# Performance work log

Hardware: AMD Instinct MI355X
Metric: run time of the kernel (lower is better)

The kernel has to match this reference:

```python
import jax, jax.numpy as jnp
import numpy as np

V = 131072          # total vertices (hits) across all events
K = 64              # neighbours per vertex, col 0 == self
NSEG = 4            # number of events (row splits segments)
THRESHOLD = 0.5     # hierarchy score cut (layer's non-trainable threshold var)


def setup_inputs() -> dict:
    key = jax.random.key(0)
    k1, k2 = jax.random.split(key)
    score = jax.random.uniform(k1, (V, 1), dtype=jnp.float32)
    seg = V // NSEG
    base = (jnp.arange(V, dtype=jnp.int32) // seg) * seg
    # random neighbours constrained to the same segment; column 0 is self
    rnd = jax.random.randint(k2, (V, K - 1), 0, seg, dtype=jnp.int32) + base[:, None]
    nidxs = jnp.concatenate([jnp.arange(V, dtype=jnp.int32)[:, None], rnd], axis=1)
    row_splits = (jnp.arange(NSEG + 1, dtype=jnp.int32) * seg)
    return {"score": score, "nidxs": nidxs, "row_splits": row_splits}


def _local_group(score1, nidxs, row_splits, thr):
    """Greedy threshold-based neighbour grouping (HGCalML LocalGroup op).

    Vertices are visited per segment in descending score order. An unused
    vertex becomes a group seed; if its score > thr it absorbs all of its
    not-yet-used neighbours. Returns fixed-shape (-1 padded) outputs so the
    whole thing is jit-compatible.
    """
    V_, K_ = nidxs.shape
    seg_id = jnp.searchsorted(row_splits, jnp.arange(V_, dtype=row_splits.dtype),
                              side='right') - 1
    # per-segment descending-score order == tf.argsort(DESC) per row split
    order = jnp.lexsort((-score1, seg_id)).astype(jnp.int32)
    kcols = jnp.arange(K_)

    def step(state, v):
        used, assign, dirn, sel, seed, count = state
        is_new = jnp.logical_not(used[v])                 # v not grouped yet -> seed
        expand = score1[v] > thr                          # absorb neighbours?
        cand = jnp.where(expand, nidxs[v],
                         jnp.where(kcols == 0, v, -1))    # else only self
        safe = jnp.clip(cand, 0, V_ - 1)
        valid = (cand >= 0) & jnp.logical_not(used[safe]) & is_new
        used = used.at[safe].set(used[safe] | valid)
        assign = assign.at[safe].set(jnp.where(valid, count, assign[safe]))
        dirn = dirn.at[v].set(jnp.where(valid, cand, -1))
        sel = sel.at[count].set(jnp.where(is_new, v, sel[count]))
        seed = seed.at[v].set(seed[v] | is_new)
        count = count + is_new.astype(jnp.int32)
        return (used, assign, dirn, sel, seed, count), None

    init = (jnp.zeros(V_, dtype=bool),                 # used
            jnp.full(V_, -1, jnp.int32),               # backgather: seed rank per vertex
            jnp.full((V_, K_), -1, jnp.int32),         # directed neighbour idxs
            jnp.full(V_, -1, jnp.int32),               # selected seed vertices, -1 padded
            jnp.zeros(V_, dtype=bool),                 # seed mask
            jnp.int32(0))
    (used, assign, dirn, sel, seed, count), _ = jax.lax.scan(step, init, order)
    cs0 = jnp.concatenate([jnp.zeros(1, jnp.int32),
                           jnp.cumsum(seed.astype(jnp.int32))])
    rs_new = cs0[row_splits]                           # new row splits over seeds
    return rs_new, dirn, sel[:, None], assign, count


def reference(score, nidxs, row_splits):
    # layer: score = clip(score, 0, 1); per-segment argsort; LocalGroup
    score1 = jnp.clip(score.reshape(-1), 0.0, 1.0)
    rs_new, dirnidx, sel, backgather, n_sel = _local_group(score1, nidxs,
                                                           row_splits, THRESHOLD)
    # return_backscatter=True -> back = [V, sel]; we return sel (padded) + n_sel
    # outputs: directed nidx (V,K), selection idxs (V,1 padded with -1),
    #          backgather (V,), new row splits, number selected
    return dirnidx, sel, backgather, rs_new, n_sel
```

## Files before the change

### kernel.cpp

```cpp
#include <hip/hip_runtime.h>
#include <stdint.h>

#define INFU 0xFFFFFFFFu
#define LCAP 32768
#define NC 128

__global__ void __launch_bounds__(256) k_hist(const float* score, unsigned* bcnt,
                                              unsigned* claim, int* sel, int V, int SEGN){
  int v = blockIdx.x*blockDim.x+threadIdx.x; if (v>=V) return;
  claim[v]=INFU;
  sel[v]=-1;
  float s = score[v]; s = fminf(fmaxf(s,0.f),1.f);
  int b = (int)(s*(float)SEGN); if (b>=SEGN) b=SEGN-1; if (b<0) b=0;
  int bd = SEGN-1-b;
  int seg = v / SEGN;
  atomicAdd(&bcnt[(size_t)seg*SEGN+bd], 1u);
}

__global__ void __launch_bounds__(1024) k_scan(const unsigned* in, const unsigned* claim,
                                               unsigned* outExcl, unsigned* segTotal,
                                               int SEGN, int mode){
  int seg = blockIdx.x; int tid = threadIdx.x; int lane = tid&63, wv = tid>>6;
  __shared__ unsigned wsum[16];
  const int CH = (SEGN+1023)>>10;
  int i0 = tid*CH, i1 = i0+CH; if (i1>SEGN) i1=SEGN;
  const size_t base = (size_t)seg*SEGN;
  unsigned sum=0;
  for (int i=i0;i<i1;i++){
    unsigned x = (mode==0)? in[base+i] : ((claim[base+i]==INFU)?1u:0u);
    sum+=x;
  }
  unsigned incl=sum;
  for (int off=1;off<64;off<<=1){ unsigned t=__shfl_up(incl,(unsigned)off); if (lane>=off) incl+=t; }
  if (lane==63) wsum[wv]=incl;
  __syncthreads();
  unsigned wbase=0,total=0;
  for (int w=0;w<16;w++){ unsigned s=wsum[w]; if (w<wv) wbase+=s; total+=s; }
  unsigned run = wbase + incl - sum;
  for (int i=i0;i<i1;i++){
    unsigned x = (mode==0)? in[base+i] : ((claim[base+i]==INFU)?1u:0u);
    outExcl[base+i]=run; run+=x;
  }
  if (tid==0 && segTotal) segTotal[seg]=total;
}

__global__ void __launch_bounds__(256) k_scatter(const float* score, const unsigned* bbase,
                                                 unsigned* bfill, unsigned long long* slot,
                                                 int V, int SEGN){
  int v = blockIdx.x*blockDim.x+threadIdx.x; if (v>=V) return;
  float s = score[v]; s=fminf(fmaxf(s,0.f),1.f);
  int b=(int)(s*(float)SEGN); if(b>=SEGN)b=SEGN-1; if(b<0)b=0;
  int bd=SEGN-1-b; int seg=v/SEGN;
  size_t bk = (size_t)seg*SEGN+bd;
  unsigned pos = bbase[bk] + atomicAdd(&bfill[bk],1u);
  unsigned kb = ~__float_as_uint(s);
  slot[(size_t)seg*SEGN+pos] = ((unsigned long long)kb<<32) | (unsigned)v;
}

__global__ void __launch_bounds__(256) k_bsort(const unsigned* bcnt, const unsigned* bbase,
                                               unsigned long long* slot, int V, int SEGN){
  int t = blockIdx.x*blockDim.x+threadIdx.x; if (t>=V) return;
  unsigned n = bcnt[t];
  if (n<2) return;
  int seg = t / SEGN;
  unsigned long long* a = slot + (size_t)seg*SEGN + bbase[t];
  for (unsigned i=1;i<n;i++){
    unsigned long long key=a[i]; int j=(int)i-1;
    while (j>=0 && a[j]>key){ a[j+1]=a[j]; j--; }
    a[j+1]=key;
  }
}

__global__ void __launch_bounds__(256) k_build(const unsigned long long* slot,
                                               int* ord, unsigned* rnkv, int* segE,
                                               int V, int SEGN){
  int r = blockIdx.x*blockDim.x+threadIdx.x; if (r>=V) return;
  unsigned long long sl = slot[r];
  int v = (int)(unsigned)(sl & 0xFFFFFFFFull);
  ord[r]=v;
  int seg = r / SEGN; int rl = r - seg*SEGN;
  rnkv[v] = (unsigned)rl;
  float s = __uint_as_float(~(unsigned)(sl>>32));
  bool ex = (s > 0.5f);
  if (rl==0 && !ex) segE[seg]=0;
  if (ex){
    if (rl==SEGN-1) segE[seg]=SEGN;
    else {
      float s2 = __uint_as_float(~(unsigned)(slot[r+1]>>32));
      if (!(s2 > 0.5f)) segE[seg]=rl+1;
    }
  }
}

__global__ void __launch_bounds__(256) k_pack4(const int* ord, const unsigned* rnkv, const int* nidxs,
                                               const int* segE, unsigned short* nbr16,
                                               int V, int K, int SEGN){
  const int K4 = K>>2;
  long long q = (long long)blockIdx.x*256 + threadIdx.x;
  if (q >= (long long)V*K4) return;
  int gr = (int)(q / K4); int k4 = (int)(q - (long long)gr*K4);
  int seg = gr / SEGN, r = gr - seg*SEGN;
  if (r >= segE[seg]) return;
  int v = ord[gr];
  const int4 nn = *(const int4*)(nidxs + (size_t)v*K + (size_t)k4*4);
  ushort4 o;
  o.x=(unsigned short)rnkv[nn.x]; o.y=(unsigned short)rnkv[nn.y];
  o.z=(unsigned short)rnkv[nn.z]; o.w=(unsigned short)rnkv[nn.w];
  *(ushort4*)(nbr16 + (size_t)gr*K + (size_t)k4*4) = o;
}
__global__ void __launch_bounds__(256) k_pack(const int* ord, const unsigned* rnkv, const int* nidxs,
                                              const int* segE, unsigned short* nbr16,
                                              int V, int K, int SEGN){
  long long t = (long long)blockIdx.x*256 + threadIdx.x;
  if (t >= (long long)V*K) return;
  int gr = (int)(t / K); int k = (int)(t - (long long)gr*K);
  int seg = gr / SEGN, r = gr - seg*SEGN;
  if (r >= segE[seg]) return;
  int v = ord[gr];
  int w = nidxs[(size_t)v*K + k];
  nbr16[t] = (unsigned short)rnkv[w];
}

__global__ void __launch_bounds__(1024) k_greedy(const unsigned short* nbr16, const int* segE,
                                                 unsigned* claim, int SEGN, int K){
  __shared__ unsigned s_cl[LCAP/2];
  __shared__ unsigned char s_pos[LCAP];
  __shared__ unsigned s_cand[NC];
  __shared__ unsigned long long s_McLo[NC];
  __shared__ unsigned long long s_McHi[NC];
  __shared__ unsigned long long s_anyLo, s_anyHi;
  __shared__ unsigned long long s_bm[16];
  __shared__ unsigned s_wcur;
  __shared__ unsigned long long s_v0, s_v1;
  const int seg = blockIdx.x, tid = threadIdx.x, lane = tid&63, wv = tid>>6;
  unsigned* clg = claim + (size_t)seg*SEGN;
  const int E = segE[seg];
  const int cap = (LCAP < SEGN) ? LCAP : SEGN;
  const int capw = (cap+1)>>1;
  for (int i=tid; i<capw; i+=1024) s_cl[i]=0xFFFFFFFFu;
  for (int i=tid; i<((cap+3)>>2); i+=1024) ((unsigned*)s_pos)[i]=0u;
  if (tid<NC) s_cand[tid]=INFU;
  const unsigned long long lt_mask = (lane==0) ? 0ull : ((~0ull) >> (64-lane));
  unsigned wcursor = 0;
  for (;;){
    __syncthreads();
    if (tid<NC){
      unsigned pc = s_cand[tid];
      if (pc!=INFU && pc<(unsigned)cap) s_pos[pc]=0;
      s_cand[tid]=INFU; s_McLo[tid]=0ull; s_McHi[tid]=0ull;
    }
    if (tid==NC)   s_anyLo=0ull;
    if (tid==NC+1) s_anyHi=0ull;
    int found = 0;
    for (;;){
      unsigned r = wcursor + (unsigned)(wv*64 + lane);
      bool undec=false;
      if (r<(unsigned)E){
        if (r<(unsigned)cap)
          undec = (((s_cl[r>>1]>>((r&1)*16))&0xFFFFu)==0xFFFFu);
        else
          undec = (__hip_atomic_load(&clg[r], __ATOMIC_RELAXED, __HIP_MEMORY_SCOPE_AGENT)==INFU);
      }
      unsigned long long m = __ballot(undec);
      if (lane==0) s_bm[wv]=m;
      __syncthreads();
      unsigned long long mb = (lane<16)? s_bm[lane] : 0ull;
      int pc16 = (int)__popcll(mb);
      int incl = pc16;
      #pragma unroll
      for (int off=1; off<16; off<<=1){ int t=__shfl_up(incl,off); if (lane>=off) incl+=t; }
      int total = __shfl(incl, 15);
      int below = __shfl(incl, wv) - __shfl(pc16, wv);
      int pos = found + below + (int)__popcll(m & lt_mask);
      if (undec && pos<NC){
        s_cand[pos]=r;
        if (r<(unsigned)cap) s_pos[r]=(unsigned char)(pos+1);
      }
      if (undec && pos==NC-1) s_wcur=r+1;
      bool filled = (found+total>=NC);
      bool winend = (wcursor + 1024 >= (unsigned)E);
      __syncthreads();
      if (filled){ wcursor = s_wcur; found=NC; break; }
      found += total;
      if (winend){ wcursor=(unsigned)E; break; }
      wcursor += 1024;
    }
    const int ncand = found;
    if (!ncand) break;
    unsigned rwq[8], cq[8];
    #pragma unroll
    for (int q=0;q<8;q++){
      int c=(wv<<3)|q;
      cq[q] = (c<ncand) ? s_cand[c] : INFU;
    }
    #pragma unroll
    for (int q=0;q<8;q++){
      rwq[q]=INFU;
      if (cq[q]!=INFU && lane<K)
        rwq[q] = (unsigned)nbr16[((size_t)seg*SEGN + cq[q])*K + lane];
    }
    const bool fastmap = (s_cand[ncand-1] < (unsigned)cap);
    #pragma unroll
    for (int q=0;q<8;q++){
      int c=(wv<<3)|q;
      if (cq[q]!=INFU){
        unsigned rw = rwq[q];
        int p = -1;
        if (fastmap){
          if (rw<(unsigned)cap){ p = (int)s_pos[rw] - 1; }
        } else {
          int pp=0;
          if (s_cand[pp+64]<=rw) pp+=64;
          if (s_cand[pp+32]<=rw) pp+=32;
          if (s_cand[pp+16]<=rw) pp+=16;
          if (s_cand[pp+8 ]<=rw) pp+=8;
          if (s_cand[pp+4 ]<=rw) pp+=4;
          if (s_cand[pp+2 ]<=rw) pp+=2;
          if (s_cand[pp+1 ]<=rw) pp+=1;
          if (pp<ncand && s_cand[pp]==rw) p=pp;
        }
        if (lane<K && p>c){
          if (p<64){ atomicOr(&s_McLo[c], 1ull<<p);      atomicOr(&s_anyLo, 1ull<<p); }
          else     { atomicOr(&s_McHi[c], 1ull<<(p-64)); atomicOr(&s_anyHi, 1ull<<(p-64)); }
        }
      }
    }
    __syncthreads();
    if (wv==0){
      const int n0 = (ncand<64)? ncand : 64;
      const int n1 = ncand - n0;
      const unsigned long long nmask0 = (n0==64)? ~0ull : ((1ull<<n0)-1ull);
      unsigned long long Mj0 = s_McLo[lane];
      unsigned long long any0 = s_anyLo & nmask0;
      unsigned long long valid0 = (~any0) & nmask0;
      unsigned long long rem = any0;
      while (rem){
        int i=__builtin_ctzll(rem); rem &= rem-1;
        bool pred = ((valid0>>lane)&1ull) && (lane<i) && ((Mj0>>i)&1ull);
        if (__ballot(pred)==0ull) valid0 |= (1ull<<i);
      }
      unsigned long long valid1 = 0ull;
      if (n1>0){
        const unsigned long long nmask1 = (n1==64)? ~0ull : ((1ull<<n1)-1ull);
        unsigned long long sp = ((valid0>>lane)&1ull) ? s_McHi[lane] : 0ull;
        #pragma unroll
        for (int off=32; off; off>>=1)
          sp |= (unsigned long long)__shfl_xor((long long)sp, off);
        unsigned long long Mj1 = s_McHi[64+lane];
        unsigned long long any1 = s_anyHi & nmask1;
        valid1 = (~(any1|sp)) & nmask1;
        unsigned long long rem1 = any1 & ~sp;
        while (rem1){
          int i=__builtin_ctzll(rem1); rem1 &= rem1-1;
          bool pred = ((valid1>>lane)&1ull) && (lane<i) && ((Mj1>>i)&1ull);
          if (__ballot(pred)==0ull) valid1 |= (1ull<<i);
        }
      }
      if (lane==0){ s_v0=valid0; s_v1=valid1; }
    }
    __syncthreads();
    const unsigned long long v0 = s_v0, v1 = s_v1;
    #pragma unroll
    for (int q=0;q<8;q++){
      int c=(wv<<3)|q;
      bool isv = (c<64) ? (((v0>>c)&1ull)!=0ull) : (((v1>>(c-64))&1ull)!=0ull);
      if (cq[q]!=INFU && isv){
        unsigned rw=rwq[q], cr=cq[q];
        if (rw>cr && rw!=INFU){
          if (rw<(unsigned)cap){
            unsigned idx=rw>>1, sh=(rw&1)*16;
            unsigned old=s_cl[idx];
            for(;;){
              unsigned curv=(old>>sh)&0xFFFFu;
              if (cr>=curv) break;
              unsigned neu=(old & ~(0xFFFFu<<sh)) | (cr<<sh);
              unsigned prev=atomicCAS(&s_cl[idx], old, neu);
              if (prev==old) break;
              old=prev;
            }
          } else {
            atomicMin(&clg[rw], cr);
          }
        }
      }
    }
  }
  __syncthreads();
  for (int r=tid; r<cap; r+=1024){
    unsigned c=(s_cl[r>>1]>>((r&1)*16))&0xFFFFu;
    clg[r] = (c==0xFFFFu) ? INFU : c;
  }
}

__global__ void __launch_bounds__(256) k_absorb(const unsigned* rnkv, const unsigned* claim,
                                                unsigned* absorb, int V, int SEGN){
  int v = blockIdx.x*blockDim.x+threadIdx.x; if (v>=V) return;
  int seg = v / SEGN;
  unsigned r = rnkv[v];
  unsigned c = claim[(size_t)seg*SEGN + r];
  absorb[v] = (c==INFU)? r : c;
}

__global__ void __launch_bounds__(256) k_dirnAll4(const int* nidxs, const unsigned* rnkv,
                                                  const unsigned* absorb, const float* score,
                                                  const unsigned* segTotal,
                                                  const unsigned* srank,
                                                  int* dirn, int* sel, int* backg,
                                                  int* rs, int* nsel,
                                                  int V, int K, int SEGN, int NSEG){
  const int K4 = K>>2;
  long long q = (long long)blockIdx.x*256 + threadIdx.x;
  if (q >= (long long)V*K4) return;
  int v = (int)(q / K4); int k4 = (int)(q - (long long)v*K4);
  int seg = v / SEGN;
  if (q <= (long long)NSEG){
    unsigned run=0;
    for (int s=0;s<(int)q;s++) run+=segTotal[s];
    rs[q]=(int)run;
    if ((int)q==NSEG) nsel[0]=(int)run;
  }
  unsigned r = rnkv[v];
  unsigned a_self = absorb[v];
  bool seed = (a_self == r);
  if (k4==0){
    unsigned segOff=0;
    for (int s=0;s<seg;s++) segOff+=segTotal[s];
    unsigned g = segOff + srank[(size_t)seg*SEGN + a_self];
    backg[v] = (int)g;
    if (seed) sel[g] = v;
  }
  int4 o = make_int4(-1,-1,-1,-1);
  if (seed){
    float s = score[v]; s=fminf(fmaxf(s,0.f),1.f);
    if (!(s > 0.5f)){
      if (k4==0) o.x = v;
    } else {
      const int4 nn = *(const int4*)(nidxs + (size_t)v*K + (size_t)k4*4);
      if (absorb[nn.x]==r) o.x=nn.x;
      if (absorb[nn.y]==r) o.y=nn.y;
      if (absorb[nn.z]==r) o.z=nn.z;
      if (absorb[nn.w]==r) o.w=nn.w;
    }
  }
  *(int4*)(dirn + (size_t)v*K + (size_t)k4*4) = o;
}
__global__ void __launch_bounds__(256) k_dirnAll(const int* nidxs, const unsigned* rnkv,
                                                 const unsigned* absorb, const float* score,
                                                 const unsigned* segTotal,
                                                 const unsigned* srank,
                                                 int* dirn, int* sel, int* backg,
                                                 int* rs, int* nsel,
                                                 int V, int K, int SEGN, int NSEG){
  long long t = (long long)blockIdx.x*blockDim.x + threadIdx.x;
  if (t >= (long long)V*K) return;
  int v = (int)(t / K); int j = (int)(t - (long long)v*K);
  int seg = v / SEGN;
  if (t <= (long long)NSEG){
    unsigned run=0;
    for (int s=0;s<(int)t;s++) run+=segTotal[s];
    rs[t]=(int)run;
    if ((int)t==NSEG) nsel[0]=(int)run;
  }
  unsigned r = rnkv[v];
  unsigned a_self = absorb[v];
  bool seed = (a_self == r);
  if (j==0){
    unsigned segOff=0;
    for (int s=0;s<seg;s++) segOff+=segTotal[s];
    unsigned g = segOff + srank[(size_t)seg*SEGN + a_self];
    backg[v] = (int)g;
    if (seed) sel[g] = v;
  }
  int out = -1;
  if (seed){
    float s = score[v]; s=fminf(fmaxf(s,0.f),1.f);
    if (!(s > 0.5f)){
      out = (j==0)? v : -1;
    } else {
      int w = nidxs[(size_t)v*K + j];
      out = (absorb[w] == r)? w : -1;
    }
  }
  dirn[t] = out;
}

extern "C" void kernel_launch(void* const* d_in, const int* in_sizes, int n_in,
                              void* d_out, int out_size, void* d_ws, size_t ws_size,
                              hipStream_t stream) {
  const float* score   = (const float*)d_in[0];
  const int*   nidxs   = (const int*)d_in[1];
  (void)d_in[2];

  const int V    = in_sizes[0];
  const int K    = in_sizes[1] / V;
  const int NSEG = in_sizes[2] - 1;
  const int SEGN = V / NSEG;

  char* w = (char*)d_ws;
  unsigned long long* slot = (unsigned long long*)w;  w += (size_t)V*8;
  unsigned* bcnt  = (unsigned*)w; w += (size_t)V*4;
  unsigned* bfill = (unsigned*)w; w += (size_t)V*4;
  unsigned* bbase = (unsigned*)w; w += (size_t)V*4;
  int*      ord   = (int*)w;      w += (size_t)V*4;
  unsigned* rnkv  = (unsigned*)w; w += (size_t)V*4;
  unsigned* claim = (unsigned*)w; w += (size_t)V*4;
  unsigned* srank = (unsigned*)w; w += (size_t)V*4;
  unsigned* segTotal = (unsigned*)w; w += 64;
  int*      segE     = (int*)w;      w += 64;
  unsigned* absorb = bcnt;

  int* out      = (int*)d_out;
  int* out_dirn = out;
  int* out_sel  = out + (size_t)V*K;
  int* out_bg   = out_sel + V;
  int* out_rs   = out_bg + V;
  int* out_nsel = out_rs + (NSEG+1);

  unsigned short* nbr16 = (unsigned short*)out_dirn;

  hipMemsetAsync(bcnt,  0x00, (size_t)V*8, stream);

  int nb256 = (V + 255)/256;
  long long totVK = (long long)V*K;
  int nbVK = (int)((totVK + 255)/256);
  const bool vec4 = (K>=4) && ((K&3)==0);
  int nbQ = (int)(((long long)V*(K>>2) + 255)/256);

  k_hist<<<nb256, 256, 0, stream>>>(score, bcnt, claim, out_sel, V, SEGN);
  k_scan<<<NSEG, 1024, 0, stream>>>(bcnt, nullptr, bbase, nullptr, SEGN, 0);
  k_scatter<<<nb256, 256, 0, stream>>>(score, bbase, bfill, slot, V, SEGN);
  k_bsort<<<nb256, 256, 0, stream>>>(bcnt, bbase, slot, V, SEGN);
  k_build<<<nb256, 256, 0, stream>>>(slot, ord, rnkv, segE, V, SEGN);
  if (vec4) k_pack4<<<nbQ, 256, 0, stream>>>(ord, rnkv, nidxs, segE, nbr16, V, K, SEGN);
  else      k_pack <<<nbVK, 256, 0, stream>>>(ord, rnkv, nidxs, segE, nbr16, V, K, SEGN);
  k_greedy<<<NSEG, 1024, 0, stream>>>(nbr16, segE, claim, SEGN, K);
  k_scan<<<NSEG, 1024, 0, stream>>>(nullptr, claim, srank, segTotal, SEGN, 1);
  k_absorb<<<nb256, 256, 0, stream>>>(rnkv, claim, absorb, V, SEGN);
  if (vec4) k_dirnAll4<<<nbQ, 256, 0, stream>>>(nidxs, rnkv, absorb, score, segTotal, srank,
                                                out_dirn, out_sel, out_bg, out_rs, out_nsel,
                                                V, K, SEGN, NSEG);
  else      k_dirnAll<<<nbVK, 256, 0, stream>>>(nidxs, rnkv, absorb, score, segTotal, srank,
                                                out_dirn, out_sel, out_bg, out_rs, out_nsel,
                                                V, K, SEGN, NSEG);
}
```

Baseline: 367.8 us.

## Fuse neighbour packing, seed scan and absorb into greedy kernel

Removes the pre-pass that packed neighbour ranks into a 16-bit buffer. The greedy kernel now gathers nidxs and rnkv directly for each candidate. The greedy kernel's epilogue also computes the seed prefix ranks, segment totals and absorb array when the segment fits in shared memory, so the separate scan and absorb launches are skipped. This saves a full V*K pass and two launches. In exchange the serial greedy loop does a double-indirect gather from global memory with 32-bit reads, which raises latency on the critical single-block-per-segment path.

```diff
diff --git a/kernel.cpp b/kernel.cpp
--- a/kernel.cpp
+++ b/kernel.cpp
@@ -92,37 +92,11 @@
   }
 }
 
-__global__ void __launch_bounds__(256) k_pack4(const int* ord, const unsigned* rnkv, const int* nidxs,
-                                               const int* segE, unsigned short* nbr16,
-                                               int V, int K, int SEGN){
-  const int K4 = K>>2;
-  long long q = (long long)blockIdx.x*256 + threadIdx.x;
-  if (q >= (long long)V*K4) return;
-  int gr = (int)(q / K4); int k4 = (int)(q - (long long)gr*K4);
-  int seg = gr / SEGN, r = gr - seg*SEGN;
-  if (r >= segE[seg]) return;
-  int v = ord[gr];
-  const int4 nn = *(const int4*)(nidxs + (size_t)v*K + (size_t)k4*4);
-  ushort4 o;
-  o.x=(unsigned short)rnkv[nn.x]; o.y=(unsigned short)rnkv[nn.y];
-  o.z=(unsigned short)rnkv[nn.z]; o.w=(unsigned short)rnkv[nn.w];
-  *(ushort4*)(nbr16 + (size_t)gr*K + (size_t)k4*4) = o;
-}
-__global__ void __launch_bounds__(256) k_pack(const int* ord, const unsigned* rnkv, const int* nidxs,
-                                              const int* segE, unsigned short* nbr16,
-                                              int V, int K, int SEGN){
-  long long t = (long long)blockIdx.x*256 + threadIdx.x;
-  if (t >= (long long)V*K) return;
-  int gr = (int)(t / K); int k = (int)(t - (long long)gr*K);
-  int seg = gr / SEGN, r = gr - seg*SEGN;
-  if (r >= segE[seg]) return;
-  int v = ord[gr];
-  int w = nidxs[(size_t)v*K + k];
-  nbr16[t] = (unsigned short)rnkv[w];
-}
-
-__global__ void __launch_bounds__(1024) k_greedy(const unsigned short* nbr16, const int* segE,
-                                                 unsigned* claim, int SEGN, int K){
+__global__ void __launch_bounds__(1024) k_greedy(const int* nidxs, const int* ord,
+                                                 const unsigned* rnkv, const int* segE,
+                                                 unsigned* claim, unsigned* srank,
+                                                 unsigned* segTotal, unsigned* absorb,
+                                                 int SEGN, int K){
   __shared__ unsigned s_cl[LCAP/2];
   __shared__ unsigned char s_pos[LCAP];
   __shared__ unsigned s_cand[NC];
@@ -130,10 +104,12 @@
   __shared__ unsigned long long s_McHi[NC];
   __shared__ unsigned long long s_anyLo, s_anyHi;
   __shared__ unsigned long long s_bm[16];
+  __shared__ unsigned s_ws[16];
   __shared__ unsigned s_wcur;
   __shared__ unsigned long long s_v0, s_v1;
   const int seg = blockIdx.x, tid = threadIdx.x, lane = tid&63, wv = tid>>6;
   unsigned* clg = claim + (size_t)seg*SEGN;
+  const size_t segbase = (size_t)seg*SEGN;
   const int E = segE[seg];
   const int cap = (LCAP < SEGN) ? LCAP : SEGN;
   const int capw = (cap+1)>>1;
@@ -187,7 +163,7 @@
     }
     const int ncand = found;
     if (!ncand) break;
-    unsigned rwq[8], cq[8];
+    unsigned rwq[8], cq[8]; int vq[8];
     #pragma unroll
     for (int q=0;q<8;q++){
       int c=(wv<<3)|q;
@@ -195,9 +171,14 @@
     }
     #pragma unroll
     for (int q=0;q<8;q++){
+      vq[q] = 0;
+      if (cq[q]!=INFU) vq[q] = ord[segbase + cq[q]];
+    }
+    #pragma unroll
+    for (int q=0;q<8;q++){
       rwq[q]=INFU;
       if (cq[q]!=INFU && lane<K)
-        rwq[q] = (unsigned)nbr16[((size_t)seg*SEGN + cq[q])*K + lane];
+        rwq[q] = rnkv[ nidxs[(size_t)vq[q]*K + lane] ];
     }
     const bool fastmap = (s_cand[ncand-1] < (unsigned)cap);
     #pragma unroll
@@ -286,9 +267,37 @@
     }
   }
   __syncthreads();
-  for (int r=tid; r<cap; r+=1024){
-    unsigned c=(s_cl[r>>1]>>((r&1)*16))&0xFFFFu;
-    clg[r] = (c==0xFFFFu) ? INFU : c;
+  if (cap == SEGN){
+    const int CH2 = (((cap + 1023) >> 10) | 1);
+    int i0 = tid*CH2; if (i0>cap) i0=cap;
+    int i1 = i0+CH2;  if (i1>cap) i1=cap;
+    unsigned cnt=0;
+    for (int i=i0;i<i1;i++){
+      unsigned c=(s_cl[i>>1]>>((i&1)*16))&0xFFFFu;
+      cnt += (c==0xFFFFu)?1u:0u;
+    }
+    unsigned incl=cnt;
+    for (int off=1;off<64;off<<=1){ unsigned t2=__shfl_up(incl,(unsigned)off); if (lane>=off) incl+=t2; }
+    if (lane==63) s_ws[wv]=incl;
+    __syncthreads();
+    unsigned wbase=0,total=0;
+    for (int w2=0;w2<16;w2++){ unsigned s2=s_ws[w2]; if (w2<wv) wbase+=s2; total+=s2; }
+    unsigned run = wbase + incl - cnt;
+    for (int i=i0;i<i1;i++){
+      unsigned c=(s_cl[i>>1]>>((i&1)*16))&0xFFFFu;
+      bool isSeed = (c==0xFFFFu);
+      srank[segbase + i] = run;
+      run += isSeed?1u:0u;
+      clg[i] = isSeed ? INFU : c;
+      int v2 = ord[segbase + i];
+      absorb[v2] = isSeed ? (unsigned)i : c;
+    }
+    if (tid==0) segTotal[seg]=total;
+  } else {
+    for (int r=tid; r<cap; r+=1024){
+      unsigned c=(s_cl[r>>1]>>((r&1)*16))&0xFFFFu;
+      clg[r] = (c==0xFFFFu) ? INFU : c;
+    }
   }
 }
 
@@ -416,8 +425,6 @@
   int* out_rs   = out_bg + V;
   int* out_nsel = out_rs + (NSEG+1);
 
-  unsigned short* nbr16 = (unsigned short*)out_dirn;
-
   hipMemsetAsync(bcnt,  0x00, (size_t)V*8, stream);
 
   int nb256 = (V + 255)/256;
@@ -431,11 +438,12 @@
   k_scatter<<<nb256, 256, 0, stream>>>(score, bbase, bfill, slot, V, SEGN);
   k_bsort<<<nb256, 256, 0, stream>>>(bcnt, bbase, slot, V, SEGN);
   k_build<<<nb256, 256, 0, stream>>>(slot, ord, rnkv, segE, V, SEGN);
-  if (vec4) k_pack4<<<nbQ, 256, 0, stream>>>(ord, rnkv, nidxs, segE, nbr16, V, K, SEGN);
-  else      k_pack <<<nbVK, 256, 0, stream>>>(ord, rnkv, nidxs, segE, nbr16, V, K, SEGN);
-  k_greedy<<<NSEG, 1024, 0, stream>>>(nbr16, segE, claim, SEGN, K);
-  k_scan<<<NSEG, 1024, 0, stream>>>(nullptr, claim, srank, segTotal, SEGN, 1);
-  k_absorb<<<nb256, 256, 0, stream>>>(rnkv, claim, absorb, V, SEGN);
+  k_greedy<<<NSEG, 1024, 0, stream>>>(nidxs, ord, rnkv, segE, claim, srank, segTotal, absorb,
+                                      SEGN, K);
+  if (SEGN > LCAP){
+    k_scan<<<NSEG, 1024, 0, stream>>>(nullptr, claim, srank, segTotal, SEGN, 1);
+    k_absorb<<<nb256, 256, 0, stream>>>(rnkv, claim, absorb, V, SEGN);
+  }
   if (vec4) k_dirnAll4<<<nbQ, 256, 0, stream>>>(nidxs, rnkv, absorb, score, segTotal, srank,
                                                 out_dirn, out_sel, out_bg, out_rs, out_nsel,
                                                 V, K, SEGN, NSEG);
```

Measured after the change: 453.5 us. +23.3%, slower.
